# Kernel optimization log

Hardware: AMD Instinct MI355X
Metric: run time of the kernel (lower is better)

Reference implementation:

```python
import jax, jax.numpy as jnp
import numpy as np

ALPHA = 0.1
BETA = 0.3
MARGIN = 2.0


def setup_inputs() -> dict:
    key = jax.random.key(0)
    k1, k2 = jax.random.split(key)
    prediction = jax.random.normal(k1, (8, 2048, 512), dtype=jnp.float32)
    target_seg = jax.random.randint(k2, (8, 2048), 0, 16, dtype=jnp.int64)
    return {"prediction": prediction, "target_seg": target_seg}


def _pairwise_sqdist(x):
    # x: [n, L, d] -> squared Euclidean distances [n, L, L] via a GEMM
    sq = jnp.sum(x * x, axis=-1)  # [n, L]
    inner = jnp.einsum('nld,nmd->nlm', x, x)  # [n, L, L]
    d2 = sq[:, :, None] + sq[:, None, :] - 2.0 * inner
    return jnp.maximum(d2, 0.0)


def _safe_sqrt(d2):
    # sqrt with zero (not NaN) gradient at 0, matching torch.cdist behavior
    pos = d2 > 0
    return jnp.where(pos, jnp.sqrt(jnp.where(pos, d2, 1.0)), 0.0)


def reference(prediction, target_seg):
    # y[i,j,k] = 1 if target_seg[i,j] == target_seg[i,k]
    y = (target_seg[:, :, None] == target_seg[:, None, :]).astype(prediction.dtype)
    d2 = _pairwise_sqdist(prediction)
    dist = _safe_sqrt(d2)
    hinge = jnp.maximum(MARGIN - dist, 0.0)
    loss = ALPHA * y * d2 + BETA * (1.0 - y) * hinge * hinge
    return jnp.mean(loss)
```

## Files before the change

### kernel.cpp

```cpp
#include <hip/hip_runtime.h>
#include <hip/hip_fp8.h>
#include <math.h>

#define L      2048
#define DDIM   512
#define NBATCH 8
#define NTILE  16
#define NPAIR  (NTILE * (NTILE + 1) / 2)
#define SCREEN_BLOCKS (NBATCH * NPAIR)

#define ALPHA  0.1
#define BETA   0.3
#define PAN2   2048

typedef __attribute__((ext_vector_type(16))) float f32x16;
typedef long long2v __attribute__((ext_vector_type(2)));

__global__ __launch_bounds__(256) void gsum_kernel(const float* __restrict__ pred,
                                                   const int*   __restrict__ seg,
                                                   float* __restrict__ Spart,
                                                   float* __restrict__ Tpart) {
    __shared__ float Sl[8][16][32];
    __shared__ float Tl[8][16][32];
    int bid = blockIdx.x;
    int n   = bid & 7;
    int c   = (bid >> 3) & 15;
    int qtr = bid >> 7;
    int t = threadIdx.x;
    int d = t & 31, p = t >> 5;

    for (int i = t; i < 8 * 16 * 32; i += 256) {
        ((float*)Sl)[i] = 0.0f;
        ((float*)Tl)[i] = 0.0f;
    }
    __syncthreads();

    const float* pb   = pred + (size_t)n * L * DDIM + c * 32 + d;
    const int*   segb = seg + n * L + qtr * 512;
    #pragma unroll 4
    for (int i = 0; i < 64; ++i) {
        int lr  = i * 8 + p;
        int row = qtr * 512 + lr;
        float x = pb[(size_t)row * DDIM];
        int g   = segb[lr];
        Sl[p][g][d] += x;
        Tl[p][g][d] += x * x;
    }
    __syncthreads();

    for (int i = t; i < 512; i += 256) {
        int g = i >> 5, dd = i & 31;
        float s = 0.0f, tt = 0.0f;
        #pragma unroll
        for (int q = 0; q < 8; ++q) { s += Sl[q][g][dd]; tt += Tl[q][g][dd]; }
        Spart[((size_t)bid * 16 + g) * 32 + dd] = s;
        Sl[0][g][dd] = tt;
    }
    __syncthreads();
    if (t < 16) {
        float tt = 0.0f;
        #pragma unroll
        for (int dd = 0; dd < 32; ++dd) tt += Sl[0][t][dd];
        Tpart[bid * 16 + t] = tt;
    }
}

__global__ __launch_bounds__(256) void conv64_kernel(const float* __restrict__ pred,
                                                     unsigned char* __restrict__ h8,
                                                     float* __restrict__ sq64,
                                                     float* __restrict__ n64) {
    int t    = threadIdx.x;
    int rowl = t >> 3;
    int d8   = t & 7;
    int row  = blockIdx.x * 32 + rowl;
    const float* p = pred + (size_t)row * DDIM + d8 * 8;
    float4 v0 = *(const float4*)(p);
    float4 v1 = *(const float4*)(p + 4);
    float vals[8] = {v0.x, v0.y, v0.z, v0.w, v1.x, v1.y, v1.z, v1.w};
    unsigned q[8];
    float s = 0.0f;
    #pragma unroll
    for (int i = 0; i < 8; ++i) {
        float x = vals[i];
        s = fmaf(x, x, s);
        __hip_fp8_e4m3 f8(x);
        q[i] = (unsigned)f8.__x;
    }
    unsigned lo = q[0] | (q[1] << 8) | (q[2] << 16) | (q[3] << 24);
    unsigned hi = q[4] | (q[5] << 8) | (q[6] << 16) | (q[7] << 24);
    int pair  = d8 >> 2;
    int kodd  = (d8 >> 1) & 1;
    int khalf = d8 & 1;
    size_t off = (size_t)blockIdx.x * PAN2 + pair * 1024
               + ((row & 31) + 32 * khalf) * 16 + kodd * 8;
    *(uint2*)(h8 + off) = make_uint2(lo, hi);
    s += __shfl_down(s, 4);
    s += __shfl_down(s, 2);
    s += __shfl_down(s, 1);
    if (d8 == 0) { sq64[row] = s; n64[row] = sqrtf(s); }
}

__global__ __launch_bounds__(256) void screen_kernel(
        const unsigned char* __restrict__ h8,
        const float* __restrict__ sq64,
        const float* __restrict__ n64,
        const int*   __restrict__ seg,
        const float* __restrict__ pred,
        double* __restrict__ hpart) {
    __shared__ double wred[4];
    int bid = blockIdx.x;
    int n = bid & 7;
    int p = bid >> 3;
    int tj = 0;
    while (true) {
        int rl2 = NTILE - tj;
        if (p < rl2) break;
        p -= rl2;
        ++tj;
    }
    int tk = tj + p;

    int t    = threadIdx.x;
    int wid  = t >> 6;
    int lane = t & 63;
    int wr   = wid >> 1, wc = wid & 1;
    int l31  = lane & 31;
    int hsel = lane >> 5;

    const unsigned char* pa0 = h8 + (size_t)(n * 64 + tj * 4 + wr * 2 + 0) * PAN2 + lane * 16;
    const unsigned char* pa1 = pa0 + PAN2;
    const unsigned char* pb0 = h8 + (size_t)(n * 64 + tk * 4 + wc * 2 + 0) * PAN2 + lane * 16;
    const unsigned char* pb1 = pb0 + PAN2;

    f32x16 acc[2][2];
    #pragma unroll
    for (int m = 0; m < 2; ++m)
        #pragma unroll
        for (int nf = 0; nf < 2; ++nf)
            #pragma unroll
            for (int x = 0; x < 16; ++x) acc[m][nf][x] = 0.0f;

    #pragma unroll
    for (int ks2 = 0; ks2 < 2; ++ks2) {
        long2v a0 = *(const long2v*)(pa0 + ks2 * 1024);
        long2v a1 = *(const long2v*)(pa1 + ks2 * 1024);
        long2v b0 = *(const long2v*)(pb0 + ks2 * 1024);
        long2v b1 = *(const long2v*)(pb1 + ks2 * 1024);
        acc[0][0] = __builtin_amdgcn_mfma_f32_32x32x16_fp8_fp8(a0.x, b0.x, acc[0][0], 0, 0, 0);
        acc[0][1] = __builtin_amdgcn_mfma_f32_32x32x16_fp8_fp8(a0.x, b1.x, acc[0][1], 0, 0, 0);
        acc[1][0] = __builtin_amdgcn_mfma_f32_32x32x16_fp8_fp8(a1.x, b0.x, acc[1][0], 0, 0, 0);
        acc[1][1] = __builtin_amdgcn_mfma_f32_32x32x16_fp8_fp8(a1.x, b1.x, acc[1][1], 0, 0, 0);
        acc[0][0] = __builtin_amdgcn_mfma_f32_32x32x16_fp8_fp8(a0.y, b0.y, acc[0][0], 0, 0, 0);
        acc[0][1] = __builtin_amdgcn_mfma_f32_32x32x16_fp8_fp8(a0.y, b1.y, acc[0][1], 0, 0, 0);
        acc[1][0] = __builtin_amdgcn_mfma_f32_32x32x16_fp8_fp8(a1.y, b0.y, acc[1][0], 0, 0, 0);
        acc[1][1] = __builtin_amdgcn_mfma_f32_32x32x16_fp8_fp8(a1.y, b1.y, acc[1][1], 0, 0, 0);
    }

    const int*   segb = seg + n * L;
    const float* sqb  = sq64 + n * L;
    const float* nb   = n64 + n * L;

    double hsum = 0.0;
    #pragma unroll
    for (int nf = 0; nf < 2; ++nf) {
        int k = tk * 128 + wc * 64 + nf * 32 + l31;
        float sqk = sqb[k];
        float nk  = nb[k];
        int   sgk = segb[k];
        #pragma unroll
        for (int m = 0; m < 2; ++m)
            #pragma unroll
            for (int x = 0; x < 16; ++x) {
                int j = tj * 128 + wr * 64 + m * 32 + (x & 3) + 8 * (x >> 2) + 4 * hsel;
                if (j >= k) continue;
                if (segb[j] == sgk) continue;
                float d2e = sqb[j] + sqk - 2.0f * acc[m][nf][x];
                float thr = 4.5f + 0.27f * nb[j] * nk;
                if (d2e >= thr) continue;
                const float* pj  = pred + (size_t)(n * L + j) * DDIM;
                const float* pk2 = pred + (size_t)(n * L + k) * DDIM;
                float d2x = 0.0f;
                for (int d = 0; d < DDIM; ++d) {
                    float df = pj[d] - pk2[d];
                    d2x = fmaf(df, df, d2x);
                }
                if (d2x < 4.0f) {
                    float dist = sqrtf(d2x);
                    float hg = 2.0f - dist;
                    hsum += (double)hg * (double)hg * 2.0;
                }
            }
    }

    #pragma unroll
    for (int off = 32; off > 0; off >>= 1)
        hsum += __shfl_down(hsum, off);
    if (lane == 0) wred[wid] = hsum;
    __syncthreads();
    if (t == 0) hpart[bid] = (wred[0] + wred[1]) + (wred[2] + wred[3]);
}

__global__ __launch_bounds__(256) void pergroup_kernel(const float* __restrict__ Spart,
                                                       const float* __restrict__ Tpart,
                                                       const int*   __restrict__ seg,
                                                       double* __restrict__ gval) {
    __shared__ double red[256];
    __shared__ int cl[64];
    int bid = blockIdx.x;
    int n = bid >> 4, g = bid & 15;
    int t = threadIdx.x;

    const int* segb = seg + n * L;
    int cnt = 0;
    for (int i = t; i < L; i += 256) cnt += (segb[i] == g);
    #pragma unroll
    for (int off = 32; off > 0; off >>= 1) cnt += __shfl_down(cnt, off);
    if ((t & 63) == 0) cl[t >> 6] = cnt;
    __syncthreads();
    int c_g = cl[0] + cl[1] + cl[2] + cl[3];

    double a = 0.0;
    for (int dg = t; dg < 512; dg += 256) {
        int c = dg >> 5, dd = dg & 31;
        float s = 0.0f;
        #pragma unroll
        for (int q = 0; q < 4; ++q)
            s += Spart[((size_t)(q * 128 + c * 8 + n) * 16 + g) * 32 + dd];
        a -= 2.0 * (double)s * (double)s;
    }
    if (t < 64) {
        int q = t >> 4, c = t & 15;
        a += 2.0 * (double)c_g * (double)Tpart[(q * 128 + c * 8 + n) * 16 + g];
    }
    red[t] = a;
    __syncthreads();
    #pragma unroll
    for (int s2 = 128; s2 > 0; s2 >>= 1) {
        if (t < s2) red[t] += red[t + s2];
        __syncthreads();
    }
    if (t == 0) gval[bid] = red[0];
}

__global__ __launch_bounds__(256) void final_kernel(const double* __restrict__ gval,
                                                    const double* __restrict__ hpart,
                                                    float* __restrict__ out) {
    __shared__ double red[256];
    int t = threadIdx.x;
    double a = 0.0;
    if (t < 128) a = ALPHA * gval[t];
    for (int i = t; i < SCREEN_BLOCKS; i += 256) a += BETA * hpart[i];
    red[t] = a;
    __syncthreads();
    #pragma unroll
    for (int s2 = 128; s2 > 0; s2 >>= 1) {
        if (t < s2) red[t] += red[t + s2];
        __syncthreads();
    }
    if (t == 0)
        out[0] = (float)(red[0] / ((double)NBATCH * (double)L * (double)L));
}

extern "C" void kernel_launch(void* const* d_in, const int* in_sizes, int n_in,
                              void* d_out, int out_size, void* d_ws, size_t ws_size,
                              hipStream_t stream) {
    const float* pred = (const float*)d_in[0];
    const int*   seg  = (const int*)d_in[1];
    float* out = (float*)d_out;

    unsigned char* h8   = (unsigned char*)d_ws;
    float* sq64         = (float*)(h8 + 512 * PAN2);
    float* n64          = sq64 + NBATCH * L;
    float* Spart        = n64 + NBATCH * L;
    float* Tpart        = Spart + 512 * 16 * 32;
    double* hpart       = (double*)(Tpart + 512 * 16);
    double* gval        = hpart + SCREEN_BLOCKS;

    gsum_kernel<<<512, 256, 0, stream>>>(pred, seg, Spart, Tpart);
    conv64_kernel<<<512, 256, 0, stream>>>(pred, h8, sq64, n64);
    screen_kernel<<<SCREEN_BLOCKS, 256, 0, stream>>>(h8, sq64, n64, seg, pred, hpart);
    pergroup_kernel<<<128, 256, 0, stream>>>(Spart, Tpart, seg, gval);
    final_kernel<<<1, 256, 0, stream>>>(gval, hpart, out);
}
```

Before: 55.92 us.

## Fuse fp8 packing and row norms into group-sum kernel, drop conv64 pass

The separate conv64 kernel is removed. Its fp8 quantization and squared-norm work moves into the group-sum kernel, where blocks covering the first 64 feature columns stage fp8 bytes and partial norms in shared memory and then write the MFMA panel layout. Per-group sums are now kept in registers with predicated adds, replacing shared-memory read-modify-write. The screen kernel combines the two partial norms and takes square roots in shared memory. This saves one launch and one full read of the prediction tensor, at the cost of more shared memory and register pressure in the fused kernel and uneven work across its blocks.

```diff
diff --git a/kernel.cpp b/kernel.cpp
--- a/kernel.cpp
+++ b/kernel.cpp
@@ -12,16 +12,22 @@
 #define ALPHA  0.1
 #define BETA   0.3
 #define PAN2   2048
+#define NL     (NBATCH * L)
 
 typedef __attribute__((ext_vector_type(16))) float f32x16;
 typedef long long2v __attribute__((ext_vector_type(2)));
 
-__global__ __launch_bounds__(256) void gsum_kernel(const float* __restrict__ pred,
-                                                   const int*   __restrict__ seg,
-                                                   float* __restrict__ Spart,
-                                                   float* __restrict__ Tpart) {
+__global__ __launch_bounds__(256) void fused_kernel(const float* __restrict__ pred,
+                                                    const int*   __restrict__ seg,
+                                                    float* __restrict__ Spart,
+                                                    float* __restrict__ Tpart,
+                                                    float* __restrict__ sqh,
+                                                    unsigned char* __restrict__ h8) {
     __shared__ float Sl[8][16][32];
     __shared__ float Tl[8][16][32];
+    __shared__ unsigned char f8l[512][32];
+    __shared__ float sql[512];
+
     int bid = blockIdx.x;
     int n   = bid & 7;
     int c   = (bid >> 3) & 15;
@@ -29,22 +35,40 @@
     int t = threadIdx.x;
     int d = t & 31, p = t >> 5;
 
-    for (int i = t; i < 8 * 16 * 32; i += 256) {
-        ((float*)Sl)[i] = 0.0f;
-        ((float*)Tl)[i] = 0.0f;
-    }
-    __syncthreads();
+    float sacc[16], tacc[16];
+    #pragma unroll
+    for (int g = 0; g < 16; ++g) { sacc[g] = 0.0f; tacc[g] = 0.0f; }
 
     const float* pb   = pred + (size_t)n * L * DDIM + c * 32 + d;
     const int*   segb = seg + n * L + qtr * 512;
-    #pragma unroll 4
+    const bool packer = (c < 2);
+
+    #pragma unroll 2
     for (int i = 0; i < 64; ++i) {
         int lr  = i * 8 + p;
-        int row = qtr * 512 + lr;
-        float x = pb[(size_t)row * DDIM];
+        float x = pb[(size_t)(qtr * 512 + lr) * DDIM];
         int g   = segb[lr];
-        Sl[p][g][d] += x;
-        Tl[p][g][d] += x * x;
+        float x2 = x * x;
+        #pragma unroll
+        for (int gg = 0; gg < 16; ++gg) {
+            bool sel = (g == gg);
+            sacc[gg] += sel ? x : 0.0f;
+            tacc[gg] += sel ? x2 : 0.0f;
+        }
+        if (packer) {
+            __hip_fp8_e4m3 f8(x);
+            f8l[lr][d] = f8.__x;
+            float rs = x2;
+            #pragma unroll
+            for (int off = 16; off > 0; off >>= 1) rs += __shfl_xor(rs, off, 32);
+            if (d == 0) sql[lr] = rs;
+        }
+    }
+
+    #pragma unroll
+    for (int gg = 0; gg < 16; ++gg) {
+        Sl[p][gg][d] = sacc[gg];
+        Tl[p][gg][d] = tacc[gg];
     }
     __syncthreads();
 
@@ -63,51 +87,33 @@
         for (int dd = 0; dd < 32; ++dd) tt += Sl[0][t][dd];
         Tpart[bid * 16 + t] = tt;
     }
-}
-
-__global__ __launch_bounds__(256) void conv64_kernel(const float* __restrict__ pred,
-                                                     unsigned char* __restrict__ h8,
-                                                     float* __restrict__ sq64,
-                                                     float* __restrict__ n64) {
-    int t    = threadIdx.x;
-    int rowl = t >> 3;
-    int d8   = t & 7;
-    int row  = blockIdx.x * 32 + rowl;
-    const float* p = pred + (size_t)row * DDIM + d8 * 8;
-    float4 v0 = *(const float4*)(p);
-    float4 v1 = *(const float4*)(p + 4);
-    float vals[8] = {v0.x, v0.y, v0.z, v0.w, v1.x, v1.y, v1.z, v1.w};
-    unsigned q[8];
-    float s = 0.0f;
-    #pragma unroll
-    for (int i = 0; i < 8; ++i) {
-        float x = vals[i];
-        s = fmaf(x, x, s);
-        __hip_fp8_e4m3 f8(x);
-        q[i] = (unsigned)f8.__x;
-    }
-    unsigned lo = q[0] | (q[1] << 8) | (q[2] << 16) | (q[3] << 24);
-    unsigned hi = q[4] | (q[5] << 8) | (q[6] << 16) | (q[7] << 24);
-    int pair  = d8 >> 2;
-    int kodd  = (d8 >> 1) & 1;
-    int khalf = d8 & 1;
-    size_t off = (size_t)blockIdx.x * PAN2 + pair * 1024
-               + ((row & 31) + 32 * khalf) * 16 + kodd * 8;
-    *(uint2*)(h8 + off) = make_uint2(lo, hi);
-    s += __shfl_down(s, 4);
-    s += __shfl_down(s, 2);
-    s += __shfl_down(s, 1);
-    if (d8 == 0) { sq64[row] = s; n64[row] = sqrtf(s); }
+
+    if (packer) {
+        for (int u = t; u < 2048; u += 256) {
+            int pn    = u >> 7;
+            int r5    = (u >> 2) & 31;
+            int kodd  = (u >> 1) & 1;
+            int khalf = u & 1;
+            const unsigned char* src = &f8l[pn * 32 + r5][(kodd * 2 + khalf) * 8];
+            size_t off = (size_t)(n * 64 + qtr * 16 + pn) * PAN2 + c * 1024
+                       + (r5 + 32 * khalf) * 16 + kodd * 8;
+            *(unsigned long long*)(h8 + off) = *(const unsigned long long*)src;
+        }
+        float* sqdst = sqh + (size_t)c * NL + n * L + qtr * 512;
+        for (int r = t; r < 512; r += 256) sqdst[r] = sql[r];
+    }
 }
 
 __global__ __launch_bounds__(256) void screen_kernel(
         const unsigned char* __restrict__ h8,
-        const float* __restrict__ sq64,
-        const float* __restrict__ n64,
+        const float* __restrict__ sqh,
         const int*   __restrict__ seg,
         const float* __restrict__ pred,
         double* __restrict__ hpart) {
+    __shared__ float sqn[256];
+    __shared__ float nn[256];
     __shared__ double wred[4];
+
     int bid = blockIdx.x;
     int n = bid & 7;
     int p = bid >> 3;
@@ -126,6 +132,14 @@
     int wr   = wid >> 1, wc = wid & 1;
     int l31  = lane & 31;
     int hsel = lane >> 5;
+
+    {
+        int r   = (t < 128) ? (tj * 128 + t) : (tk * 128 + (t - 128));
+        float s = sqh[(size_t)n * L + r] + sqh[(size_t)NL + n * L + r];
+        sqn[t] = s;
+        nn[t]  = sqrtf(s);
+    }
+    __syncthreads();
 
     const unsigned char* pa0 = h8 + (size_t)(n * 64 + tj * 4 + wr * 2 + 0) * PAN2 + lane * 16;
     const unsigned char* pa1 = pa0 + PAN2;
@@ -156,32 +170,32 @@
         acc[1][1] = __builtin_amdgcn_mfma_f32_32x32x16_fp8_fp8(a1.y, b1.y, acc[1][1], 0, 0, 0);
     }
 
-    const int*   segb = seg + n * L;
-    const float* sqb  = sq64 + n * L;
-    const float* nb   = n64 + n * L;
+    const int* segb = seg + n * L;
 
     double hsum = 0.0;
     #pragma unroll
     for (int nf = 0; nf < 2; ++nf) {
-        int k = tk * 128 + wc * 64 + nf * 32 + l31;
-        float sqk = sqb[k];
-        float nk  = nb[k];
+        int kl = wc * 64 + nf * 32 + l31;
+        int k  = tk * 128 + kl;
+        float sqk = sqn[128 + kl];
+        float nk  = nn[128 + kl];
         int   sgk = segb[k];
         #pragma unroll
         for (int m = 0; m < 2; ++m)
             #pragma unroll
             for (int x = 0; x < 16; ++x) {
-                int j = tj * 128 + wr * 64 + m * 32 + (x & 3) + 8 * (x >> 2) + 4 * hsel;
+                int jl = wr * 64 + m * 32 + (x & 3) + 8 * (x >> 2) + 4 * hsel;
+                int j  = tj * 128 + jl;
                 if (j >= k) continue;
                 if (segb[j] == sgk) continue;
-                float d2e = sqb[j] + sqk - 2.0f * acc[m][nf][x];
-                float thr = 4.5f + 0.27f * nb[j] * nk;
+                float d2e = sqn[jl] + sqk - 2.0f * acc[m][nf][x];
+                float thr = 4.5f + 0.27f * nn[jl] * nk;
                 if (d2e >= thr) continue;
                 const float* pj  = pred + (size_t)(n * L + j) * DDIM;
                 const float* pk2 = pred + (size_t)(n * L + k) * DDIM;
                 float d2x = 0.0f;
-                for (int d = 0; d < DDIM; ++d) {
-                    float df = pj[d] - pk2[d];
+                for (int dd = 0; dd < DDIM; ++dd) {
+                    float df = pj[dd] - pk2[dd];
                     d2x = fmaf(df, df, d2x);
                 }
                 if (d2x < 4.0f) {
@@ -205,7 +219,7 @@
                                                        const int*   __restrict__ seg,
                                                        double* __restrict__ gval) {
     __shared__ double red[256];
-    __shared__ int cl[64];
+    __shared__ int cl[4];
     int bid = blockIdx.x;
     int n = bid >> 4, g = bid & 15;
     int t = threadIdx.x;
@@ -268,17 +282,15 @@
     const int*   seg  = (const int*)d_in[1];
     float* out = (float*)d_out;
 
-    unsigned char* h8   = (unsigned char*)d_ws;
-    float* sq64         = (float*)(h8 + 512 * PAN2);
-    float* n64          = sq64 + NBATCH * L;
-    float* Spart        = n64 + NBATCH * L;
-    float* Tpart        = Spart + 512 * 16 * 32;
-    double* hpart       = (double*)(Tpart + 512 * 16);
-    double* gval        = hpart + SCREEN_BLOCKS;
-
-    gsum_kernel<<<512, 256, 0, stream>>>(pred, seg, Spart, Tpart);
-    conv64_kernel<<<512, 256, 0, stream>>>(pred, h8, sq64, n64);
-    screen_kernel<<<SCREEN_BLOCKS, 256, 0, stream>>>(h8, sq64, n64, seg, pred, hpart);
+    unsigned char* h8 = (unsigned char*)d_ws;
+    float* Spart      = (float*)(h8 + 512 * PAN2);
+    float* Tpart      = Spart + 512 * 16 * 32;
+    float* sqh        = Tpart + 512 * 16;
+    double* hpart     = (double*)(sqh + 2 * NL);
+    double* gval      = hpart + SCREEN_BLOCKS;
+
+    fused_kernel<<<512, 256, 0, stream>>>(pred, seg, Spart, Tpart, sqh, h8);
+    screen_kernel<<<SCREEN_BLOCKS, 256, 0, stream>>>(h8, sqh, seg, pred, hpart);
     pergroup_kernel<<<128, 256, 0, stream>>>(Spart, Tpart, seg, gval);
     final_kernel<<<1, 256, 0, stream>>>(gval, hpart, out);
 }
```

Measured after the change: 82.31 us. 1.47x slower.
